# Kernel optimization log

Measured on AMD Instinct MI355X. Metric: run time of the kernel, lower is better.

The kernel has to match this reference:

```python
import jax, jax.numpy as jnp
import numpy as np
import math

B, N, D, H, FFN = 4, 2048, 512, 8, 2048
DK = D // H
EPS = 1e-5


def _layer_norm(x, g, b):
    mu = jnp.mean(x, axis=-1, keepdims=True)
    var = jnp.mean((x - mu) ** 2, axis=-1, keepdims=True)
    return (x - mu) * jax.lax.rsqrt(var + EPS) * g + b


def _rotate_half(x):
    h = x.shape[-1] // 2
    return jnp.concatenate([-x[..., h:], x[..., :h]], axis=-1)


def _rope(q, k, positions):
    # q, k: (B, H, N, DK); positions: (B, N) int
    inv_freq = 1.0 / (10000.0 ** (jnp.arange(0, DK, 2, dtype=jnp.float32) / DK))  # (DK/2,)
    ang = positions[:, None, :, None].astype(jnp.float32) * inv_freq  # (B,1,N,DK/2)
    cos = jnp.concatenate([jnp.cos(ang), jnp.cos(ang)], axis=-1)  # (B,1,N,DK)
    sin = jnp.concatenate([jnp.sin(ang), jnp.sin(ang)], axis=-1)
    q = q * cos + _rotate_half(q) * sin
    k = k * cos + _rotate_half(k) * sin
    return q, k


def setup_inputs() -> dict:
    key = jax.random.key(0)
    ks = jax.random.split(key, 16)
    s = 0.02
    x = jax.random.normal(ks[0], (B, N, D), dtype=jnp.float32)
    # backward-looking hop mask within jobs: random boolean with True diagonal
    m = jax.random.uniform(ks[1], (B, N, N)) < 0.1
    o2o_mask = m | jnp.eye(N, dtype=bool)[None]
    positions = jax.random.randint(ks[2], (B, N), 0, N)
    params = {
        'wq': jax.random.normal(ks[3], (D, D)) * s, 'bq': jnp.zeros((D,)),
        'wk': jax.random.normal(ks[4], (D, D)) * s, 'bk': jnp.zeros((D,)),
        'wv': jax.random.normal(ks[5], (D, D)) * s, 'bv': jnp.zeros((D,)),
        'wo': jax.random.normal(ks[6], (D, D)) * s, 'bo': jnp.zeros((D,)),
        'ln1_g': jnp.ones((D,)), 'ln1_b': jnp.zeros((D,)),
        'ln2_g': jnp.ones((D,)), 'ln2_b': jnp.zeros((D,)),
        'w1': jax.random.normal(ks[7], (D, FFN)) * s, 'b1': jnp.zeros((FFN,)),
        'w2': jax.random.normal(ks[8], (FFN, D)) * s, 'b2': jnp.zeros((D,)),
    }
    return {'x': x, 'o2o_mask': o2o_mask, 'positions': positions, **params}


def reference(x, o2o_mask, positions, wq, bq, wk, bk, wv, bv, wo, bo,
              ln1_g, ln1_b, ln2_g, ln2_b, w1, b1, w2, b2):
    residual = x
    xn = _layer_norm(x, ln1_g, ln1_b)
    q = (xn @ wq + bq).reshape(B, N, H, DK).transpose(0, 2, 1, 3)
    k = (xn @ wk + bk).reshape(B, N, H, DK).transpose(0, 2, 1, 3)
    v = (xn @ wv + bv).reshape(B, N, H, DK).transpose(0, 2, 1, 3)
    q, k = _rope(q, k, positions)
    scores = jnp.einsum('bhqd,bhkd->bhqk', q, k) / math.sqrt(DK)
    scores = jnp.where(o2o_mask[:, None], scores, -jnp.inf)
    attn = jax.nn.softmax(scores, axis=-1)
    attn = jnp.where(jnp.isnan(attn), 0.0, attn)  # fully-masked rows -> 0
    attn_out = jnp.einsum('bhqk,bhkd->bhqd', attn, v)
    attn_out = attn_out.transpose(0, 2, 1, 3).reshape(B, N, D)
    x = residual + (attn_out @ wo + bo)
    residual = x
    h = _layer_norm(x, ln2_g, ln2_b)
    h = jax.nn.relu(h @ w1 + b1) @ w2 + b2
    return residual + h
```

## Files before the change

kernel.cpp:

```cpp
#include <hip/hip_runtime.h>
#include <hip/hip_bf16.h>
#include <math.h>

typedef __attribute__((ext_vector_type(8))) __bf16 bf16x8;
typedef __attribute__((ext_vector_type(4))) __bf16 bf16x4;
typedef __attribute__((ext_vector_type(4))) float f32x4;

#define B_ 4
#define N_ 2048
#define D_ 512
#define H_ 8
#define DK_ 64
#define F_ 2048

__device__ __forceinline__ void async16(const __bf16* g, __bf16* l) {
  __builtin_amdgcn_global_load_lds((const __attribute__((address_space(1))) void*)g,
                                   (__attribute__((address_space(3))) void*)l, 16, 0, 0);
}

__global__ __launch_bounds__(256) void prep_all(const float* __restrict__ wq,
                                                const float* __restrict__ wk,
                                                const float* __restrict__ wv,
                                                const float* __restrict__ wo,
                                                const float* __restrict__ w1,
                                                const float* __restrict__ w2,
                                                const float* __restrict__ bq,
                                                const float* __restrict__ bk,
                                                const float* __restrict__ bv,
                                                __bf16* __restrict__ wqkvt,
                                                __bf16* __restrict__ wot,
                                                __bf16* __restrict__ w1t,
                                                __bf16* __restrict__ w2t,
                                                float* __restrict__ bqkv) {
  const int id = blockIdx.x;
  if (id >= 768) {
    int i = (id - 768) * 256 + threadIdx.x;
    bqkv[i] = (i < 512) ? bq[i] : (i < 1024) ? bk[i - 512] : bv[i - 1024];
    return;
  }
  __shared__ float t[64][65];
  const float* in;
  __bf16* outp;
  int k0, n0, K, Nc;
  if (id < 256) {
    const float* src[4] = {wq, wk, wv, wo};
    __bf16* dst[4] = {wqkvt, wqkvt + 512 * 512, wqkvt + 1024 * 512, wot};
    int w = id >> 6, tl = id & 63;
    in = src[w]; outp = dst[w]; k0 = (tl & 7) * 64; n0 = (tl >> 3) * 64; K = 512; Nc = 512;
  } else if (id < 512) {
    int tl = id - 256;
    in = w1; outp = w1t; k0 = (tl & 7) * 64; n0 = (tl >> 3) * 64; K = 512; Nc = 2048;
  } else {
    int tl = id - 512;
    in = w2; outp = w2t; k0 = (tl & 31) * 64; n0 = (tl >> 5) * 64; K = 2048; Nc = 512;
  }
  const int c = threadIdx.x & 63, r4 = threadIdx.x >> 6;
#pragma unroll
  for (int p = 0; p < 16; p++) {
    int rr = p * 4 + r4;
    t[rr][c] = in[(size_t)(k0 + rr) * Nc + n0 + c];
  }
  __syncthreads();
#pragma unroll
  for (int p = 0; p < 16; p++) {
    int rr = p * 4 + r4;
    outp[(size_t)(n0 + rr) * K + k0 + c] = (__bf16)t[c][rr];
  }
}

__global__ __launch_bounds__(256) void build_bitmask(const int* __restrict__ mask,
                                                     unsigned long long* __restrict__ bm) {
  size_t t = (size_t)blockIdx.x * 256 + threadIdx.x;
  int m = mask[t];
  unsigned long long w = __ballot(m != 0);
  if ((threadIdx.x & 63) == 0) bm[t >> 6] = w;
}

__global__ __launch_bounds__(256) void ln_fwd(const float* __restrict__ x,
                                              const float* __restrict__ g,
                                              const float* __restrict__ b,
                                              __bf16* __restrict__ out) {
  int row = blockIdx.x * 4 + (threadIdx.x >> 6);
  int lane = threadIdx.x & 63;
  const float* xr = x + (size_t)row * D_ + lane * 8;
  float4 a0 = *(const float4*)xr;
  float4 a1 = *(const float4*)(xr + 4);
  float v[8] = {a0.x, a0.y, a0.z, a0.w, a1.x, a1.y, a1.z, a1.w};
  float s = 0.f;
#pragma unroll
  for (int i = 0; i < 8; i++) s += v[i];
#pragma unroll
  for (int off = 1; off < 64; off <<= 1) s += __shfl_xor(s, off);
  float mu = s * (1.f / D_);
  float q = 0.f;
#pragma unroll
  for (int i = 0; i < 8; i++) { float d = v[i] - mu; q += d * d; }
#pragma unroll
  for (int off = 1; off < 64; off <<= 1) q += __shfl_xor(q, off);
  float rs = rsqrtf(q * (1.f / D_) + 1e-5f);
  const float* gp = g + lane * 8;
  const float* bp = b + lane * 8;
  alignas(16) __bf16 o[8];
#pragma unroll
  for (int i = 0; i < 8; i++) o[i] = (__bf16)((v[i] - mu) * rs * gp[i] + bp[i]);
  *(bf16x8*)(out + (size_t)row * D_ + lane * 8) = *(bf16x8*)o;
}

__global__ __launch_bounds__(256) void rope_vtrans(const __bf16* __restrict__ qkv,
                                                   const int* __restrict__ pos,
                                                   __bf16* __restrict__ qo,
                                                   __bf16* __restrict__ ko,
                                                   __bf16* __restrict__ vt) {
  __shared__ __bf16 tl[64][65];
  const int id = blockIdx.x;
  if (id < 8192) {
    int t = id * 256 + threadIdx.x;
    int d = t & 31;
    int h = (t >> 5) & 7;
    int n = (t >> 8) & (N_ - 1);
    int b = t >> 19;
    const __bf16* base = qkv + (size_t)(b * N_ + n) * 1536 + h * 64 + d;
    float q1 = (float)base[0], q2 = (float)base[32];
    float k1 = (float)base[512], k2 = (float)base[544];
    float p = (float)pos[b * N_ + n];
    float inv = __expf(-(float)d * (9.210340371976184f / 32.f));
    float ang = p * inv;
    float sn, cs;
    sincosf(ang, &sn, &cs);
    size_t ob = ((size_t)(b * H_ + h) * N_ + n) * DK_ + d;
    qo[ob]      = (__bf16)(q1 * cs - q2 * sn);
    qo[ob + 32] = (__bf16)(q2 * cs + q1 * sn);
    ko[ob]      = (__bf16)(k1 * cs - k2 * sn);
    ko[ob + 32] = (__bf16)(k2 * cs + k1 * sn);
  } else {
    const int lin = id - 8192;
    const int n0 = (lin & 31) * 64, h = (lin >> 5) & 7, b = lin >> 8;
    const int c = threadIdx.x & 63, rr = threadIdx.x >> 6;
#pragma unroll
    for (int p = 0; p < 16; p++) {
      int i = p * 4 + rr;
      tl[i][c] = qkv[(size_t)(b * N_ + n0 + i) * 1536 + 1024 + h * 64 + c];
    }
    __syncthreads();
    size_t ob = (size_t)(b * H_ + h) * DK_ * N_;
#pragma unroll
    for (int p = 0; p < 16; p++) {
      int dd = p * 4 + rr;
      vt[ob + (size_t)dd * N_ + n0 + c] = tl[c][dd];
    }
  }
}

template <int RELU, int OBF, int RES>
__global__ __launch_bounds__(256) void gemm_bt(const __bf16* __restrict__ A,
                                               const __bf16* __restrict__ Bt,
                                               const float* __restrict__ bias,
                                               const float* __restrict__ res,
                                               void* __restrict__ Cout,
                                               int M, int N, int K) {
  __shared__ __bf16 As[128 * 32];
  __shared__ __bf16 Bs[128 * 32];
  const int tid = threadIdx.x;
  const int lane = tid & 63;
  const int wave = tid >> 6;
  const int quad = lane >> 4;
  const int l16 = lane & 15;
  const int m0 = blockIdx.y * 128;
  const int n0 = blockIdx.x * 128;
  const int wm = (wave >> 1) * 64;
  const int wn = (wave & 1) * 64;
  f32x4 acc[4][4] = {};

  const int c0 = tid, c1 = tid + 256;
  const int ar0 = c0 >> 2, ak0 = (c0 & 3) * 8;
  const int ar1 = c1 >> 2, ak1 = (c1 & 3) * 8;

  for (int k0 = 0; k0 < K; k0 += 32) {
    async16(A + (size_t)(m0 + ar0) * K + k0 + ak0, As + c0 * 8);
    async16(A + (size_t)(m0 + ar1) * K + k0 + ak1, As + c1 * 8);
    async16(Bt + (size_t)(n0 + ar0) * K + k0 + ak0, Bs + c0 * 8);
    async16(Bt + (size_t)(n0 + ar1) * K + k0 + ak1, Bs + c1 * 8);
    __syncthreads();
    bf16x8 af[4], bf[4];
#pragma unroll
    for (int mi = 0; mi < 4; mi++)
      af[mi] = *(const bf16x8*)(As + (wm + mi * 16 + l16) * 32 + quad * 8);
#pragma unroll
    for (int ni = 0; ni < 4; ni++)
      bf[ni] = *(const bf16x8*)(Bs + (wn + ni * 16 + l16) * 32 + quad * 8);
#pragma unroll
    for (int mi = 0; mi < 4; mi++)
#pragma unroll
      for (int ni = 0; ni < 4; ni++)
        acc[mi][ni] = __builtin_amdgcn_mfma_f32_16x16x32_bf16(af[mi], bf[ni], acc[mi][ni], 0, 0, 0);
    __syncthreads();
  }
#pragma unroll
  for (int ni = 0; ni < 4; ni++) {
    const int col = n0 + wn + ni * 16 + l16;
    const float bv = bias[col];
#pragma unroll
    for (int mi = 0; mi < 4; mi++) {
#pragma unroll
      for (int r = 0; r < 4; r++) {
        const int row = m0 + wm + mi * 16 + quad * 4 + r;
        float v = acc[mi][ni][r] + bv;
        if (RES) v += res[(size_t)row * N + col];
        if (RELU) v = fmaxf(v, 0.f);
        if (OBF) ((__bf16*)Cout)[(size_t)row * N + col] = (__bf16)v;
        else     ((float*)Cout)[(size_t)row * N + col] = v;
      }
    }
  }
}

template <int RELU, int OBF, int RES>
__global__ __launch_bounds__(256) void gemm_bt64(const __bf16* __restrict__ A,
                                                 const __bf16* __restrict__ Bt,
                                                 const float* __restrict__ bias,
                                                 const float* __restrict__ res,
                                                 void* __restrict__ Cout,
                                                 int M, int N, int K) {
  __shared__ __bf16 As[128 * 32];
  __shared__ __bf16 Bs[64 * 32];
  const int tid = threadIdx.x;
  const int lane = tid & 63;
  const int wave = tid >> 6;
  const int quad = lane >> 4;
  const int l16 = lane & 15;
  const int m0 = blockIdx.y * 128;
  const int n0 = blockIdx.x * 64;
  const int wm = wave * 32;
  f32x4 acc[2][4] = {};

  const int ar0 = tid >> 2, ak0 = (tid & 3) * 8;

  for (int k0 = 0; k0 < K; k0 += 32) {
    async16(A + (size_t)(m0 + ar0) * K + k0 + ak0, As + tid * 8);
    async16(A + (size_t)(m0 + 64 + ar0) * K + k0 + ak0, As + (tid + 256) * 8);
    async16(Bt + (size_t)(n0 + ar0) * K + k0 + ak0, Bs + tid * 8);
    __syncthreads();
    bf16x8 af[2], bf[4];
#pragma unroll
    for (int mi = 0; mi < 2; mi++)
      af[mi] = *(const bf16x8*)(As + (wm + mi * 16 + l16) * 32 + quad * 8);
#pragma unroll
    for (int ni = 0; ni < 4; ni++)
      bf[ni] = *(const bf16x8*)(Bs + (ni * 16 + l16) * 32 + quad * 8);
#pragma unroll
    for (int mi = 0; mi < 2; mi++)
#pragma unroll
      for (int ni = 0; ni < 4; ni++)
        acc[mi][ni] = __builtin_amdgcn_mfma_f32_16x16x32_bf16(af[mi], bf[ni], acc[mi][ni], 0, 0, 0);
    __syncthreads();
  }
#pragma unroll
  for (int ni = 0; ni < 4; ni++) {
    const int col = n0 + ni * 16 + l16;
    const float bv = bias[col];
#pragma unroll
    for (int mi = 0; mi < 2; mi++) {
#pragma unroll
      for (int r = 0; r < 4; r++) {
        const int row = m0 + wm + mi * 16 + quad * 4 + r;
        float v = acc[mi][ni][r] + bv;
        if (RES) v += res[(size_t)row * N + col];
        if (RELU) v = fmaxf(v, 0.f);
        if (OBF) ((__bf16*)Cout)[(size_t)row * N + col] = (__bf16)v;
        else     ((float*)Cout)[(size_t)row * N + col] = v;
      }
    }
  }
}

__global__ __launch_bounds__(256, 3) void flash_attn(const __bf16* __restrict__ q,
                                                     const __bf16* __restrict__ k,
                                                     const __bf16* __restrict__ vt,
                                                     const unsigned long long* __restrict__ bm,
                                                     __bf16* __restrict__ out) {
  const int qt = blockIdx.x, h = blockIdx.y, b = blockIdx.z;
  const int tid = threadIdx.x;
  const int lane = tid & 63, wave = tid >> 6;
  const int quad = lane >> 4, l16 = lane & 15;
  __shared__ __bf16 Ks[2][64 * 64];
  __shared__ __bf16 Vs[2][64 * 64];
  __shared__ __bf16 P[4][2][16 * 68];
  const size_t bh = (size_t)b * H_ + h;
  const __bf16* qp = q + (bh * N_ + qt * 128 + wave * 32) * DK_;
  const float qscale = 0.125f * 1.44269504f;
  bf16x8 qf[2][2];
#pragma unroll
  for (int s = 0; s < 2; s++)
#pragma unroll
    for (int ks = 0; ks < 2; ks++) {
      bf16x8 raw = *(const bf16x8*)(qp + (s * 16 + l16) * DK_ + ks * 32 + quad * 8);
#pragma unroll
      for (int j = 0; j < 8; j++) qf[s][ks][j] = (__bf16)((float)raw[j] * qscale);
    }
  bf16x8 onesf;
#pragma unroll
  for (int j = 0; j < 8; j++) onesf[j] = (__bf16)1.0f;

  const __bf16* kbase = k + bh * N_ * DK_;
  const __bf16* vbase = vt + bh * DK_ * N_;
  const int qrow0 = qt * 128 + wave * 32 + l16;
  const unsigned long long* bmr0 = bm + (size_t)(b * N_ + qrow0) * (N_ / 64);
  const unsigned long long* bmr1 = bmr0 + 16 * (N_ / 64);
  const int xo = l16 & 7;

  const __bf16 *kA[2], *kB[2], *vA[2], *vB[2];
#pragma unroll
  for (int bf = 0; bf < 2; bf++) {
    kA[bf] = Ks[bf] + (l16 * 8 + (quad ^ xo)) * 8;
    kB[bf] = Ks[bf] + (l16 * 8 + ((4 + quad) ^ xo)) * 8;
    vA[bf] = Vs[bf] + (l16 * 8 + (quad ^ xo)) * 8;
    vB[bf] = Vs[bf] + (l16 * 8 + ((4 + quad) ^ xo)) * 8;
  }
  __bf16* Pw[2] = {&P[wave][0][0] + l16 * 68 + quad * 4, &P[wave][1][0] + l16 * 68 + quad * 4};
  const __bf16* Pr[2] = {&P[wave][0][0] + l16 * 68 + quad * 8, &P[wave][1][0] + l16 * 68 + quad * 8};

  f32x4 oacc[2][4] = {};
  f32x4 lacc[2] = {};

  auto stage = [&](int kt, int buf) {
    const __bf16* kg = kbase + (size_t)kt * 64 * DK_;
    const __bf16* vg = vbase + kt * 64;
#pragma unroll
    for (int i = 0; i < 2; i++) {
      const int s = tid + i * 256;
      const int r = s >> 3;
      const int j = (s & 7) ^ (r & 7);
      async16(kg + r * DK_ + j * 8, Ks[buf] + s * 8);
      async16(vg + (size_t)r * N_ + j * 8, Vs[buf] + s * 8);
    }
  };

  stage(0, 0);
  unsigned long long nm0 = bmr0[0], nm1 = bmr1[0];
  __syncthreads();

  for (int kt = 0; kt < N_ / 64; kt++) {
    const int buf = kt & 1;
    if (kt + 1 < N_ / 64) stage(kt + 1, buf ^ 1);
    const unsigned long long mw0 = nm0 >> (quad * 4);
    const unsigned long long mw1 = nm1 >> (quad * 4);
    if (kt + 1 < N_ / 64) { nm0 = bmr0[kt + 1]; nm1 = bmr1[kt + 1]; }

#pragma unroll
    for (int ci = 0; ci < 4; ci++) {
      bf16x8 kf0 = *(const bf16x8*)(kA[buf] + ci * 1024);
      bf16x8 kf1 = *(const bf16x8*)(kB[buf] + ci * 1024);
#pragma unroll
      for (int s = 0; s < 2; s++) {
        f32x4 a = {0.f, 0.f, 0.f, 0.f};
        a = __builtin_amdgcn_mfma_f32_16x16x32_bf16(kf0, qf[s][0], a, 0, 0, 0);
        a = __builtin_amdgcn_mfma_f32_16x16x32_bf16(kf1, qf[s][1], a, 0, 0, 0);
        const unsigned nib = (unsigned)((s ? mw1 : mw0) >> (ci * 16)) & 15u;
        bf16x4 pk;
#pragma unroll
        for (int r = 0; r < 4; r++) {
          float in = (nib & (1u << r)) ? a[r] : -1e30f;
          pk[r] = (__bf16)exp2f(in);
        }
        *(bf16x4*)(Pw[s] + ci * 16) = pk;
      }
    }
    bf16x8 pf[2][2];
#pragma unroll
    for (int s = 0; s < 2; s++) {
      pf[s][0] = *(const bf16x8*)(Pr[s]);
      pf[s][1] = *(const bf16x8*)(Pr[s] + 32);
    }
#pragma unroll
    for (int s = 0; s < 2; s++) {
      lacc[s] = __builtin_amdgcn_mfma_f32_16x16x32_bf16(onesf, pf[s][0], lacc[s], 0, 0, 0);
      lacc[s] = __builtin_amdgcn_mfma_f32_16x16x32_bf16(onesf, pf[s][1], lacc[s], 0, 0, 0);
    }
#pragma unroll
    for (int ni = 0; ni < 4; ni++) {
      bf16x8 vf0 = *(const bf16x8*)(vA[buf] + ni * 1024);
      bf16x8 vf1 = *(const bf16x8*)(vB[buf] + ni * 1024);
#pragma unroll
      for (int s = 0; s < 2; s++) {
        oacc[s][ni] = __builtin_amdgcn_mfma_f32_16x16x32_bf16(vf0, pf[s][0], oacc[s][ni], 0, 0, 0);
        oacc[s][ni] = __builtin_amdgcn_mfma_f32_16x16x32_bf16(vf1, pf[s][1], oacc[s][ni], 0, 0, 0);
      }
    }
    __syncthreads();
  }
#pragma unroll
  for (int s = 0; s < 2; s++) {
    const float l = lacc[s][0];
    const float inv_l = (l > 0.f) ? 1.f / l : 0.f;
    const int qrow = qrow0 + s * 16;
#pragma unroll
    for (int ni = 0; ni < 4; ni++) {
      bf16x4 ov;
#pragma unroll
      for (int r = 0; r < 4; r++) ov[r] = (__bf16)(oacc[s][ni][r] * inv_l);
      *(bf16x4*)(out + ((size_t)b * N_ + qrow) * D_ + h * DK_ + ni * 16 + quad * 4) = ov;
    }
  }
}

static constexpr size_t OFF_XN  = 0;
static constexpr size_t OFF_WT  = 8388608;
static constexpr size_t OFF_WO  = OFF_WT + 1572864;
static constexpr size_t OFF_W1  = OFF_WO + 524288;
static constexpr size_t OFF_W2  = OFF_W1 + 2097152;
static constexpr size_t OFF_BQ  = OFF_W2 + 2097152;
static constexpr size_t OFF_QKV = OFF_BQ + 6144;
static constexpr size_t OFF_QR  = OFF_QKV + 25165824;
static constexpr size_t OFF_KR  = OFF_QR + 8388608;
static constexpr size_t OFF_VT  = OFF_KR + 8388608;
static constexpr size_t OFF_AO  = OFF_VT + 8388608;
static constexpr size_t OFF_Y   = OFF_AO + 8388608;

extern "C" void kernel_launch(void* const* d_in, const int* in_sizes, int n_in,
                              void* d_out, int out_size, void* d_ws, size_t ws_size,
                              hipStream_t stream) {
  const float* x    = (const float*)d_in[0];
  const int*   mask = (const int*)d_in[1];
  const int*   pos  = (const int*)d_in[2];
  const float* wq   = (const float*)d_in[3];
  const float* bq   = (const float*)d_in[4];
  const float* wk   = (const float*)d_in[5];
  const float* bk   = (const float*)d_in[6];
  const float* wv   = (const float*)d_in[7];
  const float* bv   = (const float*)d_in[8];
  const float* wo   = (const float*)d_in[9];
  const float* bo   = (const float*)d_in[10];
  const float* ln1g = (const float*)d_in[11];
  const float* ln1b = (const float*)d_in[12];
  const float* ln2g = (const float*)d_in[13];
  const float* ln2b = (const float*)d_in[14];
  const float* w1   = (const float*)d_in[15];
  const float* b1   = (const float*)d_in[16];
  const float* w2   = (const float*)d_in[17];
  const float* b2   = (const float*)d_in[18];
  float* out = (float*)d_out;
  char* ws = (char*)d_ws;

  __bf16* xn    = (__bf16*)(ws + OFF_XN);
  __bf16* wqkvt = (__bf16*)(ws + OFF_WT);
  __bf16* wot   = (__bf16*)(ws + OFF_WO);
  __bf16* w1t   = (__bf16*)(ws + OFF_W1);
  __bf16* w2t   = (__bf16*)(ws + OFF_W2);
  float*  bqkv  = (float*)(ws + OFF_BQ);
  __bf16* qkv   = (__bf16*)(ws + OFF_QKV);
  __bf16* qr    = (__bf16*)(ws + OFF_QR);
  __bf16* kr    = (__bf16*)(ws + OFF_KR);
  __bf16* vt    = (__bf16*)(ws + OFF_VT);
  __bf16* attn  = (__bf16*)(ws + OFF_AO);
  float*  y     = (float*)(ws + OFF_Y);
  unsigned long long* bm = (unsigned long long*)(ws + OFF_Y);
  __bf16* hn    = xn;
  __bf16* h2    = qkv;

  dim3 b256(256);
  prep_all<<<774, b256, 0, stream>>>(wq, wk, wv, wo, w1, w2, bq, bk, bv,
                                     wqkvt, wot, w1t, w2t, bqkv);
  build_bitmask<<<65536, b256, 0, stream>>>(mask, bm);
  ln_fwd<<<2048, b256, 0, stream>>>(x, ln1g, ln1b, xn);
  gemm_bt<0, 1, 0><<<dim3(12, 64), b256, 0, stream>>>(xn, wqkvt, bqkv, nullptr, qkv, 8192, 1536, 512);
  rope_vtrans<<<9216, b256, 0, stream>>>(qkv, pos, qr, kr, vt);
  flash_attn<<<dim3(16, 8, 4), b256, 0, stream>>>(qr, kr, vt, bm, attn);
  gemm_bt64<0, 0, 1><<<dim3(8, 64), b256, 0, stream>>>(attn, wot, bo, x, y, 8192, 512, 512);
  ln_fwd<<<2048, b256, 0, stream>>>(y, ln2g, ln2b, hn);
  gemm_bt<1, 1, 0><<<dim3(16, 64), b256, 0, stream>>>(hn, w1t, b1, nullptr, h2, 8192, 2048, 512);
  gemm_bt64<0, 0, 1><<<dim3(8, 64), b256, 0, stream>>>(h2, w2t, b2, y, out, 8192, 512, 2048);
}
```

Baseline: 402.6 us.

## Swizzle GEMM tile order and simplify flash attention row-sum and masking

The GEMM kernels now take a flat 1D grid and remap block indices into groups of 8 row tiles, so blocks that run together share A and B tiles in L2. The flash attention kernel drops its precomputed LDS pointers and its mask-word prefetch, and lowers the launch bound from 3 to 2 blocks per CU. It also replaces the ones-vector MFMA row sum with per-lane float accumulation reduced by shuffles at the end, and uses __expf with an unscaled Q instead of exp2f with a log2e-folded scale. These trade extra VALU work in the softmax loop and exposed mask-load latency for fewer MFMAs and more register headroom.

Result: faster. 389.8 us (-3.2%).

```diff
diff --git a/kernel.cpp b/kernel.cpp
--- a/kernel.cpp
+++ b/kernel.cpp
@@ -157,7 +157,7 @@
                                                const float* __restrict__ bias,
                                                const float* __restrict__ res,
                                                void* __restrict__ Cout,
-                                               int M, int N, int K) {
+                                               int M, int N, int K, int nbx) {
   __shared__ __bf16 As[128 * 32];
   __shared__ __bf16 Bs[128 * 32];
   const int tid = threadIdx.x;
@@ -165,8 +165,11 @@
   const int wave = tid >> 6;
   const int quad = lane >> 4;
   const int l16 = lane & 15;
-  const int m0 = blockIdx.y * 128;
-  const int n0 = blockIdx.x * 128;
+  const int per = nbx * 8;
+  const int sid = blockIdx.x / per;
+  const int rem = blockIdx.x % per;
+  const int m0 = (sid * 8 + (rem & 7)) * 128;
+  const int n0 = (rem >> 3) * 128;
   const int wm = (wave >> 1) * 64;
   const int wn = (wave & 1) * 64;
   f32x4 acc[4][4] = {};
@@ -220,7 +223,7 @@
                                                  const float* __restrict__ bias,
                                                  const float* __restrict__ res,
                                                  void* __restrict__ Cout,
-                                                 int M, int N, int K) {
+                                                 int M, int N, int K, int nbx) {
   __shared__ __bf16 As[128 * 32];
   __shared__ __bf16 Bs[64 * 32];
   const int tid = threadIdx.x;
@@ -228,8 +231,11 @@
   const int wave = tid >> 6;
   const int quad = lane >> 4;
   const int l16 = lane & 15;
-  const int m0 = blockIdx.y * 128;
-  const int n0 = blockIdx.x * 64;
+  const int per = nbx * 8;
+  const int sid = blockIdx.x / per;
+  const int rem = blockIdx.x % per;
+  const int m0 = (sid * 8 + (rem & 7)) * 128;
+  const int n0 = (rem >> 3) * 64;
   const int wm = wave * 32;
   f32x4 acc[2][4] = {};
 
@@ -273,7 +279,7 @@
   }
 }
 
-__global__ __launch_bounds__(256, 3) void flash_attn(const __bf16* __restrict__ q,
+__global__ __launch_bounds__(256, 2) void flash_attn(const __bf16* __restrict__ q,
                                                      const __bf16* __restrict__ k,
                                                      const __bf16* __restrict__ vt,
                                                      const unsigned long long* __restrict__ bm,
@@ -287,20 +293,15 @@
   __shared__ __bf16 P[4][2][16 * 68];
   const size_t bh = (size_t)b * H_ + h;
   const __bf16* qp = q + (bh * N_ + qt * 128 + wave * 32) * DK_;
-  const float qscale = 0.125f * 1.44269504f;
   bf16x8 qf[2][2];
 #pragma unroll
   for (int s = 0; s < 2; s++)
 #pragma unroll
     for (int ks = 0; ks < 2; ks++) {
-      bf16x8 raw = *(const bf16x8*)(qp + (s * 16 + l16) * DK_ + ks * 32 + quad * 8);
-#pragma unroll
-      for (int j = 0; j < 8; j++) qf[s][ks][j] = (__bf16)((float)raw[j] * qscale);
-    }
-  bf16x8 onesf;
-#pragma unroll
-  for (int j = 0; j < 8; j++) onesf[j] = (__bf16)1.0f;
-
+      qf[s][ks] = *(const bf16x8*)(qp + (s * 16 + l16) * DK_ + ks * 32 + quad * 8);
+#pragma unroll
+      for (int j = 0; j < 8; j++) qf[s][ks][j] = qf[s][ks][j] * (__bf16)0.125f;
+    }
   const __bf16* kbase = k + bh * N_ * DK_;
   const __bf16* vbase = vt + bh * DK_ * N_;
   const int qrow0 = qt * 128 + wave * 32 + l16;
@@ -308,19 +309,8 @@
   const unsigned long long* bmr1 = bmr0 + 16 * (N_ / 64);
   const int xo = l16 & 7;
 
-  const __bf16 *kA[2], *kB[2], *vA[2], *vB[2];
-#pragma unroll
-  for (int bf = 0; bf < 2; bf++) {
-    kA[bf] = Ks[bf] + (l16 * 8 + (quad ^ xo)) * 8;
-    kB[bf] = Ks[bf] + (l16 * 8 + ((4 + quad) ^ xo)) * 8;
-    vA[bf] = Vs[bf] + (l16 * 8 + (quad ^ xo)) * 8;
-    vB[bf] = Vs[bf] + (l16 * 8 + ((4 + quad) ^ xo)) * 8;
-  }
-  __bf16* Pw[2] = {&P[wave][0][0] + l16 * 68 + quad * 4, &P[wave][1][0] + l16 * 68 + quad * 4};
-  const __bf16* Pr[2] = {&P[wave][0][0] + l16 * 68 + quad * 8, &P[wave][1][0] + l16 * 68 + quad * 8};
-
   f32x4 oacc[2][4] = {};
-  f32x4 lacc[2] = {};
+  float lsum[2] = {0.f, 0.f};
 
   auto stage = [&](int kt, int buf) {
     const __bf16* kg = kbase + (size_t)kt * 64 * DK_;
@@ -336,50 +326,47 @@
   };
 
   stage(0, 0);
-  unsigned long long nm0 = bmr0[0], nm1 = bmr1[0];
   __syncthreads();
 
   for (int kt = 0; kt < N_ / 64; kt++) {
     const int buf = kt & 1;
     if (kt + 1 < N_ / 64) stage(kt + 1, buf ^ 1);
-    const unsigned long long mw0 = nm0 >> (quad * 4);
-    const unsigned long long mw1 = nm1 >> (quad * 4);
-    if (kt + 1 < N_ / 64) { nm0 = bmr0[kt + 1]; nm1 = bmr1[kt + 1]; }
-
+
+    const unsigned long long mw0 = bmr0[kt] >> (quad * 4);
+    const unsigned long long mw1 = bmr1[kt] >> (quad * 4);
 #pragma unroll
     for (int ci = 0; ci < 4; ci++) {
-      bf16x8 kf0 = *(const bf16x8*)(kA[buf] + ci * 1024);
-      bf16x8 kf1 = *(const bf16x8*)(kB[buf] + ci * 1024);
+      const int row = ci * 16 + l16;
+      bf16x8 kf0 = *(const bf16x8*)(Ks[buf] + (row * 8 + (quad ^ xo)) * 8);
+      bf16x8 kf1 = *(const bf16x8*)(Ks[buf] + (row * 8 + ((4 + quad) ^ xo)) * 8);
 #pragma unroll
       for (int s = 0; s < 2; s++) {
         f32x4 a = {0.f, 0.f, 0.f, 0.f};
         a = __builtin_amdgcn_mfma_f32_16x16x32_bf16(kf0, qf[s][0], a, 0, 0, 0);
         a = __builtin_amdgcn_mfma_f32_16x16x32_bf16(kf1, qf[s][1], a, 0, 0, 0);
-        const unsigned nib = (unsigned)((s ? mw1 : mw0) >> (ci * 16)) & 15u;
+        const unsigned long long mw = s ? mw1 : mw0;
         bf16x4 pk;
 #pragma unroll
         for (int r = 0; r < 4; r++) {
-          float in = (nib & (1u << r)) ? a[r] : -1e30f;
-          pk[r] = (__bf16)exp2f(in);
+          float in = ((mw >> (ci * 16 + r)) & 1ull) ? a[r] : -1e30f;
+          float p = __expf(in);
+          lsum[s] += p;
+          pk[r] = (__bf16)p;
         }
-        *(bf16x4*)(Pw[s] + ci * 16) = pk;
+        *(bf16x4*)(&P[wave][s][0] + l16 * 68 + ci * 16 + quad * 4) = pk;
       }
     }
     bf16x8 pf[2][2];
 #pragma unroll
     for (int s = 0; s < 2; s++) {
-      pf[s][0] = *(const bf16x8*)(Pr[s]);
-      pf[s][1] = *(const bf16x8*)(Pr[s] + 32);
-    }
-#pragma unroll
-    for (int s = 0; s < 2; s++) {
-      lacc[s] = __builtin_amdgcn_mfma_f32_16x16x32_bf16(onesf, pf[s][0], lacc[s], 0, 0, 0);
-      lacc[s] = __builtin_amdgcn_mfma_f32_16x16x32_bf16(onesf, pf[s][1], lacc[s], 0, 0, 0);
+      pf[s][0] = *(const bf16x8*)(&P[wave][s][0] + l16 * 68 + quad * 8);
+      pf[s][1] = *(const bf16x8*)(&P[wave][s][0] + l16 * 68 + 32 + quad * 8);
     }
 #pragma unroll
     for (int ni = 0; ni < 4; ni++) {
-      bf16x8 vf0 = *(const bf16x8*)(vA[buf] + ni * 1024);
-      bf16x8 vf1 = *(const bf16x8*)(vB[buf] + ni * 1024);
+      const int row = ni * 16 + l16;
+      bf16x8 vf0 = *(const bf16x8*)(Vs[buf] + (row * 8 + (quad ^ xo)) * 8);
+      bf16x8 vf1 = *(const bf16x8*)(Vs[buf] + (row * 8 + ((4 + quad) ^ xo)) * 8);
 #pragma unroll
       for (int s = 0; s < 2; s++) {
         oacc[s][ni] = __builtin_amdgcn_mfma_f32_16x16x32_bf16(vf0, pf[s][0], oacc[s][ni], 0, 0, 0);
@@ -390,15 +377,15 @@
   }
 #pragma unroll
   for (int s = 0; s < 2; s++) {
-    const float l = lacc[s][0];
-    const float inv_l = (l > 0.f) ? 1.f / l : 0.f;
-    const int qrow = qrow0 + s * 16;
+    lsum[s] += __shfl_xor(lsum[s], 16);
+    lsum[s] += __shfl_xor(lsum[s], 32);
+    const float inv_l = (lsum[s] > 0.f) ? 1.f / lsum[s] : 0.f;
 #pragma unroll
     for (int ni = 0; ni < 4; ni++) {
       bf16x4 ov;
 #pragma unroll
       for (int r = 0; r < 4; r++) ov[r] = (__bf16)(oacc[s][ni][r] * inv_l);
-      *(bf16x4*)(out + ((size_t)b * N_ + qrow) * D_ + h * DK_ + ni * 16 + quad * 4) = ov;
+      *(bf16x4*)(out + ((size_t)b * N_ + qrow0 + s * 16) * D_ + h * DK_ + ni * 16 + quad * 4) = ov;
     }
   }
 }
@@ -462,11 +449,11 @@
                                      wqkvt, wot, w1t, w2t, bqkv);
   build_bitmask<<<65536, b256, 0, stream>>>(mask, bm);
   ln_fwd<<<2048, b256, 0, stream>>>(x, ln1g, ln1b, xn);
-  gemm_bt<0, 1, 0><<<dim3(12, 64), b256, 0, stream>>>(xn, wqkvt, bqkv, nullptr, qkv, 8192, 1536, 512);
+  gemm_bt<0, 1, 0><<<768, b256, 0, stream>>>(xn, wqkvt, bqkv, nullptr, qkv, 8192, 1536, 512, 12);
   rope_vtrans<<<9216, b256, 0, stream>>>(qkv, pos, qr, kr, vt);
   flash_attn<<<dim3(16, 8, 4), b256, 0, stream>>>(qr, kr, vt, bm, attn);
-  gemm_bt64<0, 0, 1><<<dim3(8, 64), b256, 0, stream>>>(attn, wot, bo, x, y, 8192, 512, 512);
+  gemm_bt64<0, 0, 1><<<512, b256, 0, stream>>>(attn, wot, bo, x, y, 8192, 512, 512, 8);
   ln_fwd<<<2048, b256, 0, stream>>>(y, ln2g, ln2b, hn);
-  gemm_bt<1, 1, 0><<<dim3(16, 64), b256, 0, stream>>>(hn, w1t, b1, nullptr, h2, 8192, 2048, 512);
-  gemm_bt64<0, 0, 1><<<dim3(8, 64), b256, 0, stream>>>(h2, w2t, b2, y, out, 8192, 512, 2048);
-}
+  gemm_bt<1, 1, 0><<<1024, b256, 0, stream>>>(hn, w1t, b1, nullptr, h2, 8192, 2048, 512, 16);
+  gemm_bt64<0, 0, 1><<<512, b256, 0, stream>>>(h2, w2t, b2, y, out, 8192, 512, 2048, 8);
+}
```
